# Performance work log

Measured on AMD Instinct MI355X. Metric: run time of the kernel, lower is better.

Reference implementation:

```python
import jax, jax.numpy as jnp
import numpy as np

CHUNK_SIZE = 256


def setup_inputs() -> dict:
    key = jax.random.key(0)
    kq, kk, kv = jax.random.split(key, 3)
    b, h, L, d, dv = 2, 16, 4096, 16, 64
    return {
        "q": jax.random.normal(kq, (b, h, L, d), dtype=jnp.float32),
        "k": jax.random.normal(kk, (b, h, L, d), dtype=jnp.float32),
        "v": jax.random.normal(kv, (b, h, L, dv), dtype=jnp.float32),
    }


def reference(q, k, v):
    b, h, L, d = q.shape
    dv = v.shape[-1]
    cs = CHUNK_SIZE
    n = L // cs

    q = q * d ** (-0.5)

    # ---- normalizer z over full sequence ----
    k_cumsum = jnp.cumsum(k, axis=-2)                               # [b,h,L,d]
    kk_cumsum = jnp.cumsum(k[..., :, None] * k[..., None, :], axis=-3)  # [b,h,L,d,d]
    z = (q * k_cumsum).sum(-1)
    z = z + 0.5 * jnp.einsum('bhld,bhle,bhlde->bhl', q, q, kk_cumsum)
    z = z + (jnp.arange(L, dtype=z.dtype) + 1.0)[None, None, :]

    # ---- zeroth-order term ----
    o_const = jnp.cumsum(v, axis=-2)                                # [b,h,L,dv]

    # ---- chunked view ----
    qc = q.reshape(b, h, n, cs, d)
    kc = k.reshape(b, h, n, cs, d)
    vc = v.reshape(b, h, n, cs, dv)

    # intra-chunk quadratic attention: S + 0.5*S^2, causal-masked
    s = jnp.einsum('bhnqd,bhnkd->bhnqk', qc, kc)                    # [b,h,n,cs,cs]
    s = s + 0.5 * s ** 2
    causal_mask = jnp.tril(jnp.ones((cs, cs), dtype=bool))
    s = jnp.where(causal_mask, s, jnp.zeros((), dtype=s.dtype))
    o = jnp.einsum('bhnqk,bhnkf->bhnqf', s, vc)                     # [b,h,n,cs,dv]

    # inter-chunk quadratic state: cumulative K x K x V from previous chunks
    kv_quad = jnp.einsum('bhncd,bhnce,bhncf->bhndef', kc, kc, vc)   # [b,h,n,d,d,dv]
    kv_quad = jnp.cumsum(kv_quad, axis=2)
    kv_quad = jnp.concatenate(
        [jnp.zeros_like(kv_quad[:, :, :1]), kv_quad[:, :, :-1]], axis=2)
    o = o + 0.5 * jnp.einsum('bhndef,bhncd,bhnce->bhncf', kv_quad, qc, qc)

    # inter-chunk linear state: cumulative K x V from previous chunks
    kv_lin = jnp.einsum('bhncd,bhnce->bhnde', kc, vc)               # [b,h,n,d,dv]
    kv_lin = jnp.cumsum(kv_lin, axis=2)
    kv_lin = jnp.concatenate(
        [jnp.zeros_like(kv_lin[:, :, :1]), kv_lin[:, :, :-1]], axis=2)
    o = o + jnp.einsum('bhnde,bhncd->bhnce', kv_lin, qc)

    o = o.reshape(b, h, L, dv) + o_const
    return o / (z[..., None] + 1e-6)
```

## Files before the change

kernel.cpp:

```cpp
#include <hip/hip_runtime.h>
#include <hip/hip_cooperative_groups.h>
#include <cstddef>

#define BH    32
#define LSEQ  4096
#define D     16
#define DV    64
#define CS    256
#define NC    16
#define NF    160
#define NZ    65
#define KSTEPS 5
#define PER   (NZ * NF)

typedef short short8 __attribute__((ext_vector_type(8)));
typedef float f32x4 __attribute__((ext_vector_type(4)));
typedef float f4 __attribute__((ext_vector_type(4)));
typedef unsigned uint4v __attribute__((ext_vector_type(4)));

#define OFF_KBF 0u
#define OFF_VT  (4u*1024u*1024u)
#define OFF_ST  (OFF_VT + (unsigned)(BH*NZ*LSEQ*2))

__device__ __forceinline__ unsigned f2bf(float x) {
  unsigned u = __float_as_uint(x);
  return (u + 0x7FFFu + ((u >> 16) & 1u)) >> 16;
}
__device__ __forceinline__ float bf2f(unsigned short u) {
  return __uint_as_float(((unsigned)u) << 16);
}
__device__ __forceinline__ short8 zero8() {
  short8 z = {0,0,0,0,0,0,0,0};
  return z;
}
__device__ __forceinline__ unsigned cvtpk(float lo, float hi) {
  unsigned r;
  asm("v_cvt_pk_bf16_f32 %0, %1, %2" : "=v"(r) : "v"(lo), "v"(hi));
  return r;
}
__device__ __forceinline__ short8 pk4(unsigned a, unsigned b, unsigned c, unsigned d) {
  uint4v u = {a, b, c, d};
  return __builtin_bit_cast(short8, u);
}

__device__ __forceinline__ unsigned feat_tbl(int f) {
  if (f == 0)  return 16u | (16u << 8);
  if (f <= 16) return (unsigned)(f - 1) | (16u << 8);
  if (f < 137) {
    int p = f - 17, off = 0;
    for (int d = 0; d < 15; ++d) {
      int cnt = 15 - d;
      if (p < off + cnt) return (unsigned)d | ((unsigned)(d + 1 + p - off) << 8);
      off += cnt;
    }
  }
  if (f < 153) {
    int d = f - 137;
    return (unsigned)d | ((unsigned)d << 8) | (1u << 16);
  }
  return 17u | (17u << 8);
}

struct Smem {
  float kxqx[CS][18];
  __align__(16) unsigned short vt[NZ][264];
  union {
    __align__(16) unsigned short stt[NZ][168];
    struct {
      __align__(16) unsigned short ptile[8][640];
      float zline[CS];
    } u;
  } b;
  unsigned tbl[NF];
};

__global__ __launch_bounds__(512, 4) void unified(const float* __restrict__ q,
                                                  const float* __restrict__ k,
                                                  const float* __restrict__ v,
                                                  unsigned* __restrict__ kbf_u32,
                                                  unsigned short* __restrict__ st,
                                                  float* __restrict__ out) {
  __shared__ Smem sm;
  int blk = blockIdx.x, bh = blk >> 4, c = blk & 15;
  int t = threadIdx.x, w = t >> 6, lane = t & 63, quad = lane >> 4, n16 = lane & 15;
  const size_t base = (size_t)bh * LSEQ + (size_t)c * CS;
  (void)kbf_u32;

  const int s0 = (w < 2) ? 2 * w : (w + 2);
  const int s1 = (w < 2) ? 2 * w + 1 : (17 - w);

  short8 qf[2] = {zero8(), zero8()};
  if (quad < 2) {
#pragma unroll
    for (int mm = 0; mm < 2; ++mm) {
      int s = mm ? s1 : s0;
      const f4* qp = (const f4*)(q + (base + (size_t)(s * 16 + n16)) * D + quad * 8);
      f4 qa = qp[0] * 0.25f;
      f4 qb = qp[1] * 0.25f;
      qf[mm] = pk4(cvtpk(qa[0], qa[1]), cvtpk(qa[2], qa[3]),
                   cvtpk(qb[0], qb[1]), cvtpk(qb[2], qb[3]));
    }
  }

  {
    const f4* K4 = (const f4*)(k + base * D);
    for (int idx = t; idx < 1024; idx += 512) {
      f4 kv = K4[idx];
      float* dst = &sm.kxqx[idx >> 2][(idx & 3) * 4];
      *(float2*)dst = make_float2(kv[0], kv[1]);
      *(float2*)(dst + 2) = make_float2(kv[2], kv[3]);
    }
    for (int i = t; i < CS; i += 512)
      *(float2*)&sm.kxqx[i][16] = make_float2(1.f, 0.f);
    const f4* V4 = (const f4*)(v + base * DV);
    for (int idx = t; idx < 2048; idx += 512) {
      int m16 = idx & 15, j0 = (idx >> 4) * 2;
      f4 a  = V4[j0 * 16 + m16];
      f4 bq = V4[j0 * 16 + 16 + m16];
#pragma unroll
      for (int r = 0; r < 4; ++r)
        *(unsigned*)&sm.vt[m16 * 4 + r][j0] = cvtpk(a[r], bq[r]);
    }
    if (t < 128) ((unsigned*)&sm.vt[64][0])[t] = 0x3F803F80u;
    if (t < NF) sm.tbl[t] = feat_tbl(t);
  }
  __syncthreads();

  if (c < 15) {
    const int ntt = (w < 2) ? 2 : 1;
    unsigned short* stc = st + (size_t)(bh * NC + c) * PER;
    for (int tt = 0; tt < ntt; ++tt) {
      const int T = tt ? (w + 8) : w;
      unsigned tv = sm.tbl[T * 16 + n16];
      int d0 = tv & 255, e0 = (tv >> 8) & 255;
      f32x4 acc5[5];
#pragma unroll
      for (int nt = 0; nt < 5; ++nt) acc5[nt] = (f32x4){0.f, 0.f, 0.f, 0.f};
      for (int jt = 0; jt < 8; ++jt) {
        float x[8];
#pragma unroll
        for (int i = 0; i < 8; ++i) {
          const float* kr = &sm.kxqx[jt * 32 + quad * 8 + i][0];
          x[i] = kr[d0] * kr[e0];
        }
        short8 afr = pk4(cvtpk(x[0], x[1]), cvtpk(x[2], x[3]),
                         cvtpk(x[4], x[5]), cvtpk(x[6], x[7]));
#pragma unroll
        for (int nt = 0; nt < 5; ++nt) {
          int ncol = nt * 16 + n16;
          short8 b = zero8();
          if (ncol < NZ) b = *(const short8*)(&sm.vt[ncol][jt * 32 + quad * 8]);
          acc5[nt] = __builtin_amdgcn_mfma_f32_16x16x32_bf16(afr, b, acc5[nt], 0, 0, 0);
        }
      }
      const int feat0 = T * 16 + quad * 4;
      float sc[4];
#pragma unroll
      for (int r = 0; r < 4; ++r)
        sc[r] = (feat0 + r >= 137 && feat0 + r < 153) ? 0.5f : 1.0f;
#pragma unroll
      for (int nt = 0; nt < 5; ++nt) {
        int col = nt * 16 + n16;
        if (col < NZ) {
          unsigned lo = cvtpk(acc5[nt][0] * sc[0], acc5[nt][1] * sc[1]);
          unsigned hi = cvtpk(acc5[nt][2] * sc[2], acc5[nt][3] * sc[3]);
          *(uint2*)(stc + (size_t)col * NF + feat0) = make_uint2(lo, hi);
        }
      }
    }
  }

  f32x4 accC[2][5];
#pragma unroll
  for (int mm = 0; mm < 2; ++mm)
#pragma unroll
    for (int nt = 0; nt < 5; ++nt) accC[mm][nt] = (f32x4){0.f, 0.f, 0.f, 0.f};

  {
    unsigned short* pw = &sm.b.u.ptile[w][0];
    short8 ones;
#pragma unroll
    for (int i = 0; i < 8; ++i) ones[i] = (short)0x3F80;

#pragma unroll
    for (int mm = 0; mm < 2; ++mm) {
      const int s = mm ? s1 : s0;
      const int ntiles = (s >> 1) + 1;
      for (int jt = 0; jt < ntiles; ++jt) {
        short8 kb[2];
#pragma unroll
        for (int ntk = 0; ntk < 2; ++ntk) {
          short8 b = zero8();
          if (quad < 2) {
            const float2* kr =
                (const float2*)&sm.kxqx[jt * 32 + ntk * 16 + n16][quad * 8];
            float2 k0 = kr[0], k1 = kr[1], k2 = kr[2], k3 = kr[3];
            b = pk4(cvtpk(k0.x, k0.y), cvtpk(k1.x, k1.y),
                    cvtpk(k2.x, k2.y), cvtpk(k3.x, k3.y));
          }
          kb[ntk] = b;
        }
        f32x4 zf = (f32x4){0.f, 0.f, 0.f, 0.f};
        f32x4 sres[2];
        sres[0] = __builtin_amdgcn_mfma_f32_16x16x32_bf16(qf[mm], kb[0], zf, 0, 0, 0);
        sres[1] = __builtin_amdgcn_mfma_f32_16x16x32_bf16(qf[mm], kb[1], zf, 0, 0, 0);
        const bool last = (jt == ntiles - 1);
#pragma unroll
        for (int ntk = 0; ntk < 2; ++ntk) {
          float ph[4];
#pragma unroll
          for (int r = 0; r < 4; ++r) {
            float sv = sres[ntk][r];
            float phi = fmaf(sv, fmaf(0.5f, sv, 1.0f), 1.0f);
            if (last) {
              int qrow_g = s * 16 + quad * 4 + r;
              int kcol_g = jt * 32 + ntk * 16 + n16;
              if (kcol_g > qrow_g) phi = 0.f;
            }
            ph[r] = phi;
          }
          unsigned u01 = cvtpk(ph[0], ph[1]);
          unsigned u23 = cvtpk(ph[2], ph[3]);
          int rb = (quad * 4) * 40 + ntk * 16 + n16;
          pw[rb      ] = (unsigned short)u01;
          pw[rb +  40] = (unsigned short)(u01 >> 16);
          pw[rb +  80] = (unsigned short)u23;
          pw[rb + 120] = (unsigned short)(u23 >> 16);
        }
        short8 pa = *(const short8*)(pw + n16 * 40 + quad * 8);
#pragma unroll
        for (int nt = 0; nt < 5; ++nt) {
          int ncol = nt * 16 + n16;
          short8 b;
          if (ncol < 64)       b = *(const short8*)(&sm.vt[ncol][jt * 32 + quad * 8]);
          else if (ncol == 64) b = ones;
          else                 b = zero8();
          accC[mm][nt] = __builtin_amdgcn_mfma_f32_16x16x32_bf16(pa, b, accC[mm][nt], 0, 0, 0);
        }
      }
    }
  }
  __syncthreads();

  {
    const f4* Q4 = (const f4*)(q + base * D);
    for (int idx = t; idx < 1024; idx += 512) {
      f4 qv = Q4[idx] * 0.25f;
      float* dst = &sm.kxqx[idx >> 2][(idx & 3) * 4];
      *(float2*)dst = make_float2(qv[0], qv[1]);
      *(float2*)(dst + 2) = make_float2(qv[2], qv[3]);
    }
  }

  cooperative_groups::this_grid().sync();

  if (c > 0) {
    const unsigned short* stg = st + (size_t)bh * NC * PER;
    float sa0[8], sa1[8], sa2[8];
#pragma unroll
    for (int e = 0; e < 8; ++e) { sa0[e] = 0.f; sa1[e] = 0.f; sa2[e] = 0.f; }
    const int i0 = t * 8, i1 = i0 + 4096, i2 = i0 + 8192;
    const bool h2 = (i2 < PER);
    short8 a0 = *(const short8*)(stg + i0);
    short8 a1 = *(const short8*)(stg + i1);
    short8 a2 = h2 ? *(const short8*)(stg + i2) : zero8();
    for (int cc = 1; cc < c; ++cc) {
      const unsigned short* pn = stg + (size_t)cc * PER;
      short8 b0 = *(const short8*)(pn + i0);
      short8 b1 = *(const short8*)(pn + i1);
      short8 b2 = h2 ? *(const short8*)(pn + i2) : zero8();
#pragma unroll
      for (int e = 0; e < 8; ++e) {
        sa0[e] += bf2f((unsigned short)a0[e]);
        sa1[e] += bf2f((unsigned short)a1[e]);
        sa2[e] += bf2f((unsigned short)a2[e]);
      }
      a0 = b0; a1 = b1; a2 = b2;
    }
#pragma unroll
    for (int e = 0; e < 8; ++e) {
      sa0[e] += bf2f((unsigned short)a0[e]);
      sa1[e] += bf2f((unsigned short)a1[e]);
      sa2[e] += bf2f((unsigned short)a2[e]);
    }
    {
      int col = i0 / NF, ft = i0 - col * NF;
      *(short8*)(&sm.b.stt[col][ft]) =
          pk4(cvtpk(sa0[0], sa0[1]), cvtpk(sa0[2], sa0[3]),
              cvtpk(sa0[4], sa0[5]), cvtpk(sa0[6], sa0[7]));
      col = i1 / NF; ft = i1 - col * NF;
      *(short8*)(&sm.b.stt[col][ft]) =
          pk4(cvtpk(sa1[0], sa1[1]), cvtpk(sa1[2], sa1[3]),
              cvtpk(sa1[4], sa1[5]), cvtpk(sa1[6], sa1[7]));
      if (h2) {
        col = i2 / NF; ft = i2 - col * NF;
        *(short8*)(&sm.b.stt[col][ft]) =
            pk4(cvtpk(sa2[0], sa2[1]), cvtpk(sa2[2], sa2[3]),
                cvtpk(sa2[4], sa2[5]), cvtpk(sa2[6], sa2[7]));
      }
    }
  }
  __syncthreads();

  if (c > 0) {
    const float* qrow0 = &sm.kxqx[s0 * 16 + n16][0];
    const float* qrow1 = &sm.kxqx[s1 * 16 + n16][0];
    for (int ks = 0; ks < KSTEPS; ++ks) {
      unsigned tvv[8];
#pragma unroll
      for (int i = 0; i < 8; ++i) tvv[i] = sm.tbl[ks * 32 + quad * 8 + i];
      float x0[8], x1[8];
#pragma unroll
      for (int i = 0; i < 8; ++i) {
        int d = tvv[i] & 255, e = (tvv[i] >> 8) & 255;
        x0[i] = qrow0[d] * qrow0[e];
        x1[i] = qrow1[d] * qrow1[e];
      }
      short8 afr0 = pk4(cvtpk(x0[0], x0[1]), cvtpk(x0[2], x0[3]),
                        cvtpk(x0[4], x0[5]), cvtpk(x0[6], x0[7]));
      short8 afr1 = pk4(cvtpk(x1[0], x1[1]), cvtpk(x1[2], x1[3]),
                        cvtpk(x1[4], x1[5]), cvtpk(x1[6], x1[7]));
#pragma unroll
      for (int nt = 0; nt < 5; ++nt) {
        int ncol = nt * 16 + n16;
        short8 b = zero8();
        if (ncol < NZ) b = *(const short8*)(&sm.b.stt[ncol][ks * 32 + quad * 8]);
        accC[0][nt] = __builtin_amdgcn_mfma_f32_16x16x32_bf16(afr0, b, accC[0][nt], 0, 0, 0);
        accC[1][nt] = __builtin_amdgcn_mfma_f32_16x16x32_bf16(afr1, b, accC[1][nt], 0, 0, 0);
      }
    }
  }
  __syncthreads();

  if (n16 == 0) {
#pragma unroll
    for (int mm = 0; mm < 2; ++mm) {
      int s = mm ? s1 : s0;
#pragma unroll
      for (int r = 0; r < 4; ++r)
        sm.b.u.zline[s * 16 + quad * 4 + r] = accC[mm][4][r];
    }
  }
  float* oc = out + base * DV;
#pragma unroll
  for (int mm = 0; mm < 2; ++mm) {
    int s = mm ? s1 : s0;
#pragma unroll
    for (int r = 0; r < 4; ++r) {
      int qrow = s * 16 + quad * 4 + r;
      float inv = __builtin_amdgcn_rcpf(sm.b.u.zline[qrow] + 1e-6f);
#pragma unroll
      for (int nt = 0; nt < 4; ++nt)
        oc[(size_t)qrow * DV + nt * 16 + n16] = accC[mm][nt][r] * inv;
    }
  }
}

__global__ __launch_bounds__(320) void pass_a(const float* __restrict__ k,
                                              const float* __restrict__ v,
                                              unsigned* __restrict__ kbf_u32,
                                              unsigned* __restrict__ vt_u32,
                                              unsigned short* __restrict__ st) {
  __shared__ float kx[CS][18];
  __shared__ __align__(16) unsigned short vt_lds[NZ][264];
  __shared__ unsigned tbl[NF];
  int blk = blockIdx.x, bh = blk >> 4, c = blk & 15;
  int t = threadIdx.x, w = t >> 6, lane = t & 63, quad = lane >> 4, n16 = lane & 15;
  {
    const float2* kc2 = (const float2*)(k + ((size_t)bh * LSEQ + c * CS) * D);
    unsigned* kbd = kbf_u32 + ((size_t)bh * LSEQ + c * CS) * D / 2;
    for (int i = t; i < 2048; i += 320) {
      float2 v2 = kc2[i];
      kbd[i] = f2bf(v2.x) | (f2bf(v2.y) << 16);
      int j = i >> 3, dd = (i & 7) * 2;
      kx[j][dd] = v2.x; kx[j][dd + 1] = v2.y;
    }
    for (int i = t; i < CS; i += 320) { kx[i][16] = 1.f; kx[i][17] = 0.f; }
  }
  {
    const float* vb = v + ((size_t)bh * LSEQ + c * CS) * DV;
    for (int i = t; i < CS * DV; i += 320) {
      int j = i >> 6, f = i & 63;
      vt_lds[f][j] = (unsigned short)f2bf(vb[i]);
    }
    for (int i = t; i < CS; i += 320) vt_lds[64][i] = (unsigned short)0x3F80;
  }
  if (t < NF) tbl[t] = feat_tbl(t);
  __syncthreads();
  {
    unsigned* vtg = vt_u32 + (size_t)bh * NZ * (LSEQ / 2) + c * (CS / 2);
    for (int i = t; i < NZ * (CS / 2); i += 320) {
      int f = i >> 7, jp = (i & 127) * 2;
      vtg[(size_t)f * (LSEQ / 2) + (i & 127)] =
          (unsigned)vt_lds[f][jp] | ((unsigned)vt_lds[f][jp + 1] << 16);
    }
  }
  f32x4 acc[2][5];
#pragma unroll
  for (int mm = 0; mm < 2; ++mm)
#pragma unroll
    for (int nt = 0; nt < 5; ++nt) acc[mm][nt] = (f32x4){0.f, 0.f, 0.f, 0.f};
  for (int jt = 0; jt < 8; ++jt) {
    short8 afr[2];
#pragma unroll
    for (int mm = 0; mm < 2; ++mm) {
      int feat = (w * 2 + mm) * 16 + n16;
      unsigned tv = tbl[feat];
      int d = tv & 255, e = (tv >> 8) & 255;
      short8 a;
#pragma unroll
      for (int i = 0; i < 8; ++i) {
        int jj = jt * 32 + quad * 8 + i;
        a[i] = (short)f2bf(kx[jj][d] * kx[jj][e]);
      }
      afr[mm] = a;
    }
#pragma unroll
    for (int nt = 0; nt < 5; ++nt) {
      int ncol = nt * 16 + n16;
      short8 b = zero8();
      if (ncol < NZ) b = *(const short8*)(&vt_lds[ncol][jt * 32 + quad * 8]);
      acc[0][nt] = __builtin_amdgcn_mfma_f32_16x16x32_bf16(afr[0], b, acc[0][nt], 0, 0, 0);
      acc[1][nt] = __builtin_amdgcn_mfma_f32_16x16x32_bf16(afr[1], b, acc[1][nt], 0, 0, 0);
    }
  }
  unsigned short* stc = st + (size_t)(bh * NC + c) * PER;
#pragma unroll
  for (int mm = 0; mm < 2; ++mm)
#pragma unroll
    for (int nt = 0; nt < 5; ++nt) {
      int col = nt * 16 + n16;
      if (col < NZ) {
        unsigned lo = f2bf(acc[mm][nt][0]) | (f2bf(acc[mm][nt][1]) << 16);
        unsigned hi = f2bf(acc[mm][nt][2]) | (f2bf(acc[mm][nt][3]) << 16);
        int feat0 = (w * 2 + mm) * 16 + quad * 4;
        *(uint2*)(stc + (size_t)col * NF + feat0) = make_uint2(lo, hi);
      }
    }
}

__global__ __launch_bounds__(256) void pass_b(unsigned short* __restrict__ st) {
  const int TOT = BH * PER;
  int idx = blockIdx.x * 256 + threadIdx.x;
  if (idx >= TOT) return;
  int bh = idx / PER, r = idx - bh * PER;
  unsigned short* p = st + (size_t)bh * NC * PER + r;
  float run = 0.f;
#pragma unroll
  for (int c = 0; c < NC; ++c) {
    unsigned short uv = p[(size_t)c * PER];
    float val = bf2f(uv);
    p[(size_t)c * PER] = (unsigned short)f2bf(run);
    run += val;
  }
}

__global__ __launch_bounds__(512) void pass_c(const float* __restrict__ q,
                                              const unsigned short* __restrict__ kbf,
                                              const unsigned short* __restrict__ vt,
                                              const unsigned short* __restrict__ st,
                                              float* __restrict__ out) {
  __shared__ float qx[CS][18];
  __shared__ unsigned tbl[NF];
  __shared__ __align__(16) unsigned short ptile[8][32 * 40];
  __shared__ float zline[CS];
  int blk = blockIdx.x, bh = blk >> 4, c = blk & 15;
  const size_t base = (size_t)bh * LSEQ + (size_t)c * CS;
  const float* qc = q + base * D;
  int t = threadIdx.x, w = t >> 6, lane = t & 63, quad = lane >> 4, n16 = lane & 15;
  for (int i = t; i < CS * D; i += 512) {
    int row = i >> 4, dd = i & 15;
    qx[row][dd] = qc[i] * 0.25f;
  }
  for (int i = t; i < CS; i += 512) { qx[i][16] = 1.f; qx[i][17] = 0.f; }
  if (t < NF) tbl[t] = feat_tbl(t);
  __syncthreads();
  f32x4 acc[2][5];
#pragma unroll
  for (int mm = 0; mm < 2; ++mm)
#pragma unroll
    for (int nt = 0; nt < 5; ++nt) acc[mm][nt] = (f32x4){0.f, 0.f, 0.f, 0.f};
  if (c > 0) {
    const unsigned short* stc = st + (size_t)(bh * NC + c) * PER;
    for (int ks = 0; ks < KSTEPS; ++ks) {
      short8 afr[2];
#pragma unroll
      for (int mm = 0; mm < 2; ++mm) {
        const float* qrow = qx[(w * 2 + mm) * 16 + n16];
        short8 a;
#pragma unroll
        for (int i = 0; i < 8; ++i) {
          int f = ks * 32 + quad * 8 + i;
          unsigned tv = tbl[f];
          float val = qrow[tv & 255] * qrow[(tv >> 8) & 255];
          if (tv & 0x10000u) val *= 0.5f;
          a[i] = (short)f2bf(val);
        }
        afr[mm] = a;
      }
#pragma unroll
      for (int nt = 0; nt < 5; ++nt) {
        int ncol = nt * 16 + n16;
        short8 b = zero8();
        if (ncol < NZ) b = *(const short8*)(stc + (size_t)ncol * NF + ks * 32 + quad * 8);
        acc[0][nt] = __builtin_amdgcn_mfma_f32_16x16x32_bf16(afr[0], b, acc[0][nt], 0, 0, 0);
        acc[1][nt] = __builtin_amdgcn_mfma_f32_16x16x32_bf16(afr[1], b, acc[1][nt], 0, 0, 0);
      }
    }
  }
  short8 qfr[2];
#pragma unroll
  for (int mm = 0; mm < 2; ++mm) {
    int m = (w * 2 + mm) * 16 + n16;
    short8 a = zero8();
    if (quad < 2) {
#pragma unroll
      for (int i = 0; i < 8; ++i) a[i] = (short)f2bf(qx[m][quad * 8 + i]);
    }
    qfr[mm] = a;
  }
  const unsigned short* kbc = kbf + base * D;
  const unsigned short* vtb = vt + (size_t)bh * NZ * LSEQ + (size_t)c * CS;
  unsigned short* pw = &ptile[w][0];
  short8 ones;
#pragma unroll
  for (int i = 0; i < 8; ++i) ones[i] = (short)0x3F80;
  for (int jt = 0; jt <= w; ++jt) {
    short8 kb[2];
#pragma unroll
    for (int ntk = 0; ntk < 2; ++ntk) {
      short8 b = zero8();
      if (quad < 2)
        b = *(const short8*)(kbc + (size_t)(jt * 32 + ntk * 16 + n16) * D + quad * 8);
      kb[ntk] = b;
    }
    f32x4 zf = (f32x4){0.f, 0.f, 0.f, 0.f};
    f32x4 s[2][2];
#pragma unroll
    for (int mm = 0; mm < 2; ++mm)
#pragma unroll
      for (int ntk = 0; ntk < 2; ++ntk)
        s[mm][ntk] = __builtin_amdgcn_mfma_f32_16x16x32_bf16(qfr[mm], kb[ntk], zf, 0, 0, 0);
    bool diag = (jt == w);
#pragma unroll
    for (int mm = 0; mm < 2; ++mm)
#pragma unroll
      for (int ntk = 0; ntk < 2; ++ntk)
#pragma unroll
        for (int r = 0; r < 4; ++r) {
          float sv = s[mm][ntk][r];
          float phi = fmaf(0.5f * sv, sv, sv) + 1.0f;
          if (diag) {
            int qrow = mm * 16 + quad * 4 + r;
            int kcol = ntk * 16 + n16;
            if (kcol > qrow) phi = 0.f;
          }
          pw[(mm * 16 + quad * 4 + r) * 40 + ntk * 16 + n16] = (unsigned short)f2bf(phi);
        }
    short8 pa[2];
#pragma unroll
    for (int mm = 0; mm < 2; ++mm)
      pa[mm] = *(const short8*)(pw + (mm * 16 + n16) * 40 + quad * 8);
#pragma unroll
    for (int nt = 0; nt < 5; ++nt) {
      int ncol = nt * 16 + n16;
      short8 b;
      if (ncol < 64)       b = *(const short8*)(vtb + (size_t)ncol * LSEQ + jt * 32 + quad * 8);
      else if (ncol == 64) b = ones;
      else                 b = zero8();
      acc[0][nt] = __builtin_amdgcn_mfma_f32_16x16x32_bf16(pa[0], b, acc[0][nt], 0, 0, 0);
      acc[1][nt] = __builtin_amdgcn_mfma_f32_16x16x32_bf16(pa[1], b, acc[1][nt], 0, 0, 0);
    }
  }
  if (n16 == 0) {
#pragma unroll
    for (int mm = 0; mm < 2; ++mm)
#pragma unroll
      for (int r = 0; r < 4; ++r)
        zline[(w * 2 + mm) * 16 + quad * 4 + r] = acc[mm][4][r];
  }
  float* oc = out + base * DV;
#pragma unroll
  for (int mm = 0; mm < 2; ++mm)
#pragma unroll
    for (int r = 0; r < 4; ++r) {
      int qrow = (w * 2 + mm) * 16 + quad * 4 + r;
      float inv = 1.0f / (zline[qrow] + 1e-6f);
#pragma unroll
      for (int nt = 0; nt < 4; ++nt)
        oc[(size_t)qrow * DV + nt * 16 + n16] = acc[mm][nt][r] * inv;
    }
}

extern "C" void kernel_launch(void* const* d_in, const int* in_sizes, int n_in,
                              void* d_out, int out_size, void* d_ws, size_t ws_size,
                              hipStream_t stream) {
  (void)in_sizes; (void)n_in; (void)out_size; (void)ws_size;
  const float* q = (const float*)d_in[0];
  const float* k = (const float*)d_in[1];
  const float* v = (const float*)d_in[2];
  float* out = (float*)d_out;
  char* wsb = (char*)d_ws;
  unsigned*       kbf32 = (unsigned*)(wsb + OFF_KBF);
  unsigned short* kbf   = (unsigned short*)(wsb + OFF_KBF);
  unsigned*       vt32  = (unsigned*)(wsb + OFF_VT);
  unsigned short* vtp   = (unsigned short*)(wsb + OFF_VT);
  unsigned short* stp   = (unsigned short*)(wsb + OFF_ST);

  int nb = 0;
  hipError_t oe = hipOccupancyMaxActiveBlocksPerMultiprocessor(
      &nb, reinterpret_cast<const void*>(unified), 512, 0);
  if (oe == hipSuccess && nb >= 2) {
    void* args[] = {(void*)&q, (void*)&k, (void*)&v,
                    (void*)&kbf32, (void*)&stp, (void*)&out};
    hipLaunchCooperativeKernel(reinterpret_cast<const void*>(unified),
                               dim3(BH * NC), dim3(512), args, 0, stream);
  } else {
    pass_a<<<BH * NC, 320, 0, stream>>>(k, v, kbf32, vt32, stp);
    pass_b<<<1300, 256, 0, stream>>>(stp);
    pass_c<<<BH * NC, 512, 0, stream>>>(q, kbf, vtp, stp, out);
  }
}
```

Baseline: 134.2 us.

## Replace cooperative grid-sync kernel with two plain launches for state and output

Splits the single cooperative kernel, which used a grid-wide sync, into two ordinary kernel launches. The first builds the per-chunk bf16 K copy and the quadratic/linear state contributions. The second loads Q and V, reads the prefix of states from earlier chunks, then runs the intra-chunk causal attention using global bf16 K. Block indexing changes to bh-minor so that chunks of one head are spread across launch order. This drops cooperative launch overhead and the grid barrier, at the cost of an extra launch and of re-reading V in the second kernel.

```diff
diff --git a/kernel.cpp b/kernel.cpp
--- a/kernel.cpp
+++ b/kernel.cpp
@@ -1,5 +1,4 @@
 #include <hip/hip_runtime.h>
-#include <hip/hip_cooperative_groups.h>
 #include <cstddef>
 
 #define BH    32
@@ -19,13 +18,8 @@
 typedef unsigned uint4v __attribute__((ext_vector_type(4)));
 
 #define OFF_KBF 0u
-#define OFF_VT  (4u*1024u*1024u)
-#define OFF_ST  (OFF_VT + (unsigned)(BH*NZ*LSEQ*2))
-
-__device__ __forceinline__ unsigned f2bf(float x) {
-  unsigned u = __float_as_uint(x);
-  return (u + 0x7FFFu + ((u >> 16) & 1u)) >> 16;
-}
+#define OFF_ST  (4u*1024u*1024u)
+
 __device__ __forceinline__ float bf2f(unsigned short u) {
   return __uint_as_float(((unsigned)u) << 16);
 }
@@ -61,8 +55,92 @@
   return 17u | (17u << 8);
 }
 
-struct Smem {
-  float kxqx[CS][18];
+__global__ __launch_bounds__(512, 4) void pass1(const float* __restrict__ k,
+                                                const float* __restrict__ v,
+                                                unsigned* __restrict__ kbf_u32,
+                                                unsigned short* __restrict__ st) {
+  __shared__ float kx[CS][18];
+  __shared__ __align__(16) unsigned short vt[NZ][264];
+  __shared__ unsigned tbl[NF];
+  int blk = blockIdx.x, bh = blk & 31, c = blk >> 5;
+  int t = threadIdx.x, w = t >> 6, lane = t & 63, quad = lane >> 4, n16 = lane & 15;
+  const size_t base = (size_t)bh * LSEQ + (size_t)c * CS;
+  (void)lane;
+
+  {
+    const f4* K4 = (const f4*)(k + base * D);
+    uint2* kbd2 = (uint2*)(kbf_u32 + base * D / 2);
+    for (int idx = t; idx < 1024; idx += 512) {
+      f4 kv = K4[idx];
+      kbd2[idx] = make_uint2(cvtpk(kv[0], kv[1]), cvtpk(kv[2], kv[3]));
+      float* dst = &kx[idx >> 2][(idx & 3) * 4];
+      *(float2*)dst = make_float2(kv[0], kv[1]);
+      *(float2*)(dst + 2) = make_float2(kv[2], kv[3]);
+    }
+    for (int i = t; i < CS; i += 512) { kx[i][16] = 1.f; kx[i][17] = 0.f; }
+  }
+  if (c < 15) {
+    const f4* V4 = (const f4*)(v + base * DV);
+    for (int idx = t; idx < 2048; idx += 512) {
+      int m16 = idx & 15, j0 = (idx >> 4) * 2;
+      f4 a  = V4[j0 * 16 + m16];
+      f4 bq = V4[j0 * 16 + 16 + m16];
+#pragma unroll
+      for (int r = 0; r < 4; ++r)
+        *(unsigned*)&vt[m16 * 4 + r][j0] = cvtpk(a[r], bq[r]);
+    }
+    if (t < 128) ((unsigned*)&vt[64][0])[t] = 0x3F803F80u;
+  }
+  if (t < NF) tbl[t] = feat_tbl(t);
+  __syncthreads();
+
+  if (c < 15) {
+    const int ntt = (w < 2) ? 2 : 1;
+    unsigned short* stc = st + (size_t)(bh * NC + c) * PER;
+    for (int tt = 0; tt < ntt; ++tt) {
+      const int T = tt ? (w + 8) : w;
+      unsigned tv = tbl[T * 16 + n16];
+      int d0 = tv & 255, e0 = (tv >> 8) & 255;
+      f32x4 acc5[5];
+#pragma unroll
+      for (int nt = 0; nt < 5; ++nt) acc5[nt] = (f32x4){0.f, 0.f, 0.f, 0.f};
+      for (int jt = 0; jt < 8; ++jt) {
+        float x[8];
+#pragma unroll
+        for (int i = 0; i < 8; ++i) {
+          const float* kr = &kx[jt * 32 + quad * 8 + i][0];
+          x[i] = kr[d0] * kr[e0];
+        }
+        short8 afr = pk4(cvtpk(x[0], x[1]), cvtpk(x[2], x[3]),
+                         cvtpk(x[4], x[5]), cvtpk(x[6], x[7]));
+#pragma unroll
+        for (int nt = 0; nt < 5; ++nt) {
+          int ncol = nt * 16 + n16;
+          short8 b = zero8();
+          if (ncol < NZ) b = *(const short8*)(&vt[ncol][jt * 32 + quad * 8]);
+          acc5[nt] = __builtin_amdgcn_mfma_f32_16x16x32_bf16(afr, b, acc5[nt], 0, 0, 0);
+        }
+      }
+      const int feat0 = T * 16 + quad * 4;
+      float sc[4];
+#pragma unroll
+      for (int r = 0; r < 4; ++r)
+        sc[r] = (feat0 + r >= 137 && feat0 + r < 153) ? 0.5f : 1.0f;
+#pragma unroll
+      for (int nt = 0; nt < 5; ++nt) {
+        int col = nt * 16 + n16;
+        if (col < NZ) {
+          unsigned lo = cvtpk(acc5[nt][0] * sc[0], acc5[nt][1] * sc[1]);
+          unsigned hi = cvtpk(acc5[nt][2] * sc[2], acc5[nt][3] * sc[3]);
+          *(uint2*)(stc + (size_t)col * NF + feat0) = make_uint2(lo, hi);
+        }
+      }
+    }
+  }
+}
+
+struct Smem2 {
+  float qx[CS][18];
   __align__(16) unsigned short vt[NZ][264];
   union {
     __align__(16) unsigned short stt[NZ][168];
@@ -74,17 +152,15 @@
   unsigned tbl[NF];
 };
 
-__global__ __launch_bounds__(512, 4) void unified(const float* __restrict__ q,
-                                                  const float* __restrict__ k,
-                                                  const float* __restrict__ v,
-                                                  unsigned* __restrict__ kbf_u32,
-                                                  unsigned short* __restrict__ st,
-                                                  float* __restrict__ out) {
-  __shared__ Smem sm;
-  int blk = blockIdx.x, bh = blk >> 4, c = blk & 15;
+__global__ __launch_bounds__(512, 4) void pass2(const float* __restrict__ q,
+                                                const unsigned short* __restrict__ kbf,
+                                                const float* __restrict__ v,
+                                                const unsigned short* __restrict__ st,
+                                                float* __restrict__ out) {
+  __shared__ Smem2 sm;
+  int blk = blockIdx.x, bh = blk & 31, c = blk >> 5;
   int t = threadIdx.x, w = t >> 6, lane = t & 63, quad = lane >> 4, n16 = lane & 15;
   const size_t base = (size_t)bh * LSEQ + (size_t)c * CS;
-  (void)kbf_u32;
 
   const int s0 = (w < 2) ? 2 * w : (w + 2);
   const int s1 = (w < 2) ? 2 * w + 1 : (17 - w);
@@ -103,15 +179,14 @@
   }
 
   {
-    const f4* K4 = (const f4*)(k + base * D);
+    const f4* Q4 = (const f4*)(q + base * D);
     for (int idx = t; idx < 1024; idx += 512) {
-      f4 kv = K4[idx];
-      float* dst = &sm.kxqx[idx >> 2][(idx & 3) * 4];
-      *(float2*)dst = make_float2(kv[0], kv[1]);
-      *(float2*)(dst + 2) = make_float2(kv[2], kv[3]);
-    }
-    for (int i = t; i < CS; i += 512)
-      *(float2*)&sm.kxqx[i][16] = make_float2(1.f, 0.f);
+      f4 qv = Q4[idx] * 0.25f;
+      float* dst = &sm.qx[idx >> 2][(idx & 3) * 4];
+      *(float2*)dst = make_float2(qv[0], qv[1]);
+      *(float2*)(dst + 2) = make_float2(qv[2], qv[3]);
+    }
+    for (int i = t; i < CS; i += 512) { sm.qx[i][16] = 1.f; sm.qx[i][17] = 0.f; }
     const f4* V4 = (const f4*)(v + base * DV);
     for (int idx = t; idx < 2048; idx += 512) {
       int m16 = idx & 15, j0 = (idx >> 4) * 2;
@@ -125,134 +200,6 @@
     if (t < NF) sm.tbl[t] = feat_tbl(t);
   }
   __syncthreads();
-
-  if (c < 15) {
-    const int ntt = (w < 2) ? 2 : 1;
-    unsigned short* stc = st + (size_t)(bh * NC + c) * PER;
-    for (int tt = 0; tt < ntt; ++tt) {
-      const int T = tt ? (w + 8) : w;
-      unsigned tv = sm.tbl[T * 16 + n16];
-      int d0 = tv & 255, e0 = (tv >> 8) & 255;
-      f32x4 acc5[5];
-#pragma unroll
-      for (int nt = 0; nt < 5; ++nt) acc5[nt] = (f32x4){0.f, 0.f, 0.f, 0.f};
-      for (int jt = 0; jt < 8; ++jt) {
-        float x[8];
-#pragma unroll
-        for (int i = 0; i < 8; ++i) {
-          const float* kr = &sm.kxqx[jt * 32 + quad * 8 + i][0];
-          x[i] = kr[d0] * kr[e0];
-        }
-        short8 afr = pk4(cvtpk(x[0], x[1]), cvtpk(x[2], x[3]),
-                         cvtpk(x[4], x[5]), cvtpk(x[6], x[7]));
-#pragma unroll
-        for (int nt = 0; nt < 5; ++nt) {
-          int ncol = nt * 16 + n16;
-          short8 b = zero8();
-          if (ncol < NZ) b = *(const short8*)(&sm.vt[ncol][jt * 32 + quad * 8]);
-          acc5[nt] = __builtin_amdgcn_mfma_f32_16x16x32_bf16(afr, b, acc5[nt], 0, 0, 0);
-        }
-      }
-      const int feat0 = T * 16 + quad * 4;
-      float sc[4];
-#pragma unroll
-      for (int r = 0; r < 4; ++r)
-        sc[r] = (feat0 + r >= 137 && feat0 + r < 153) ? 0.5f : 1.0f;
-#pragma unroll
-      for (int nt = 0; nt < 5; ++nt) {
-        int col = nt * 16 + n16;
-        if (col < NZ) {
-          unsigned lo = cvtpk(acc5[nt][0] * sc[0], acc5[nt][1] * sc[1]);
-          unsigned hi = cvtpk(acc5[nt][2] * sc[2], acc5[nt][3] * sc[3]);
-          *(uint2*)(stc + (size_t)col * NF + feat0) = make_uint2(lo, hi);
-        }
-      }
-    }
-  }
-
-  f32x4 accC[2][5];
-#pragma unroll
-  for (int mm = 0; mm < 2; ++mm)
-#pragma unroll
-    for (int nt = 0; nt < 5; ++nt) accC[mm][nt] = (f32x4){0.f, 0.f, 0.f, 0.f};
-
-  {
-    unsigned short* pw = &sm.b.u.ptile[w][0];
-    short8 ones;
-#pragma unroll
-    for (int i = 0; i < 8; ++i) ones[i] = (short)0x3F80;
-
-#pragma unroll
-    for (int mm = 0; mm < 2; ++mm) {
-      const int s = mm ? s1 : s0;
-      const int ntiles = (s >> 1) + 1;
-      for (int jt = 0; jt < ntiles; ++jt) {
-        short8 kb[2];
-#pragma unroll
-        for (int ntk = 0; ntk < 2; ++ntk) {
-          short8 b = zero8();
-          if (quad < 2) {
-            const float2* kr =
-                (const float2*)&sm.kxqx[jt * 32 + ntk * 16 + n16][quad * 8];
-            float2 k0 = kr[0], k1 = kr[1], k2 = kr[2], k3 = kr[3];
-            b = pk4(cvtpk(k0.x, k0.y), cvtpk(k1.x, k1.y),
-                    cvtpk(k2.x, k2.y), cvtpk(k3.x, k3.y));
-          }
-          kb[ntk] = b;
-        }
-        f32x4 zf = (f32x4){0.f, 0.f, 0.f, 0.f};
-        f32x4 sres[2];
-        sres[0] = __builtin_amdgcn_mfma_f32_16x16x32_bf16(qf[mm], kb[0], zf, 0, 0, 0);
-        sres[1] = __builtin_amdgcn_mfma_f32_16x16x32_bf16(qf[mm], kb[1], zf, 0, 0, 0);
-        const bool last = (jt == ntiles - 1);
-#pragma unroll
-        for (int ntk = 0; ntk < 2; ++ntk) {
-          float ph[4];
-#pragma unroll
-          for (int r = 0; r < 4; ++r) {
-            float sv = sres[ntk][r];
-            float phi = fmaf(sv, fmaf(0.5f, sv, 1.0f), 1.0f);
-            if (last) {
-              int qrow_g = s * 16 + quad * 4 + r;
-              int kcol_g = jt * 32 + ntk * 16 + n16;
-              if (kcol_g > qrow_g) phi = 0.f;
-            }
-            ph[r] = phi;
-          }
-          unsigned u01 = cvtpk(ph[0], ph[1]);
-          unsigned u23 = cvtpk(ph[2], ph[3]);
-          int rb = (quad * 4) * 40 + ntk * 16 + n16;
-          pw[rb      ] = (unsigned short)u01;
-          pw[rb +  40] = (unsigned short)(u01 >> 16);
-          pw[rb +  80] = (unsigned short)u23;
-          pw[rb + 120] = (unsigned short)(u23 >> 16);
-        }
-        short8 pa = *(const short8*)(pw + n16 * 40 + quad * 8);
-#pragma unroll
-        for (int nt = 0; nt < 5; ++nt) {
-          int ncol = nt * 16 + n16;
-          short8 b;
-          if (ncol < 64)       b = *(const short8*)(&sm.vt[ncol][jt * 32 + quad * 8]);
-          else if (ncol == 64) b = ones;
-          else                 b = zero8();
-          accC[mm][nt] = __builtin_amdgcn_mfma_f32_16x16x32_bf16(pa, b, accC[mm][nt], 0, 0, 0);
-        }
-      }
-    }
-  }
-  __syncthreads();
-
-  {
-    const f4* Q4 = (const f4*)(q + base * D);
-    for (int idx = t; idx < 1024; idx += 512) {
-      f4 qv = Q4[idx] * 0.25f;
-      float* dst = &sm.kxqx[idx >> 2][(idx & 3) * 4];
-      *(float2*)dst = make_float2(qv[0], qv[1]);
-      *(float2*)(dst + 2) = make_float2(qv[2], qv[3]);
-    }
-  }
-
-  cooperative_groups::this_grid().sync();
 
   if (c > 0) {
     const unsigned short* stg = st + (size_t)bh * NC * PER;
@@ -302,9 +249,15 @@
   }
   __syncthreads();
 
+  f32x4 accC[2][5];
+#pragma unroll
+  for (int mm = 0; mm < 2; ++mm)
+#pragma unroll
+    for (int nt = 0; nt < 5; ++nt) accC[mm][nt] = (f32x4){0.f, 0.f, 0.f, 0.f};
+
   if (c > 0) {
-    const float* qrow0 = &sm.kxqx[s0 * 16 + n16][0];
-    const float* qrow1 = &sm.kxqx[s1 * 16 + n16][0];
+    const float* qrow0 = &sm.qx[s0 * 16 + n16][0];
+    const float* qrow1 = &sm.qx[s1 * 16 + n16][0];
     for (int ks = 0; ks < KSTEPS; ++ks) {
       unsigned tvv[8];
 #pragma unroll
@@ -332,6 +285,65 @@
   }
   __syncthreads();
 
+  const unsigned short* kbc = kbf + base * D;
+  unsigned short* pw = &sm.b.u.ptile[w][0];
+  short8 ones;
+#pragma unroll
+  for (int i = 0; i < 8; ++i) ones[i] = (short)0x3F80;
+
+#pragma unroll
+  for (int mm = 0; mm < 2; ++mm) {
+    const int s = mm ? s1 : s0;
+    const int ntiles = (s >> 1) + 1;
+    for (int jt = 0; jt < ntiles; ++jt) {
+      short8 kb[2];
+#pragma unroll
+      for (int ntk = 0; ntk < 2; ++ntk) {
+        short8 b = zero8();
+        if (quad < 2)
+          b = *(const short8*)(kbc + (size_t)(jt * 32 + ntk * 16 + n16) * D + quad * 8);
+        kb[ntk] = b;
+      }
+      f32x4 zf = (f32x4){0.f, 0.f, 0.f, 0.f};
+      f32x4 sres[2];
+      sres[0] = __builtin_amdgcn_mfma_f32_16x16x32_bf16(qf[mm], kb[0], zf, 0, 0, 0);
+      sres[1] = __builtin_amdgcn_mfma_f32_16x16x32_bf16(qf[mm], kb[1], zf, 0, 0, 0);
+      const bool last = (jt == ntiles - 1);
+#pragma unroll
+      for (int ntk = 0; ntk < 2; ++ntk) {
+        float ph[4];
+#pragma unroll
+        for (int r = 0; r < 4; ++r) {
+          float sv = sres[ntk][r];
+          float phi = fmaf(sv, fmaf(0.5f, sv, 1.0f), 1.0f);
+          if (last) {
+            int qrow_g = s * 16 + quad * 4 + r;
+            int kcol_g = jt * 32 + ntk * 16 + n16;
+            if (kcol_g > qrow_g) phi = 0.f;
+          }
+          ph[r] = phi;
+        }
+        unsigned u01 = cvtpk(ph[0], ph[1]);
+        unsigned u23 = cvtpk(ph[2], ph[3]);
+        int rb = (quad * 4) * 40 + ntk * 16 + n16;
+        pw[rb      ] = (unsigned short)u01;
+        pw[rb +  40] = (unsigned short)(u01 >> 16);
+        pw[rb +  80] = (unsigned short)u23;
+        pw[rb + 120] = (unsigned short)(u23 >> 16);
+      }
+      short8 pa = *(const short8*)(pw + n16 * 40 + quad * 8);
+#pragma unroll
+      for (int nt = 0; nt < 5; ++nt) {
+        int ncol = nt * 16 + n16;
+        short8 b;
+        if (ncol < 64)       b = *(const short8*)(&sm.vt[ncol][jt * 32 + quad * 8]);
+        else if (ncol == 64) b = ones;
+        else                 b = zero8();
+        accC[mm][nt] = __builtin_amdgcn_mfma_f32_16x16x32_bf16(pa, b, accC[mm][nt], 0, 0, 0);
+      }
+    }
+  }
+
   if (n16 == 0) {
 #pragma unroll
     for (int mm = 0; mm < 2; ++mm) {
@@ -354,242 +366,6 @@
         oc[(size_t)qrow * DV + nt * 16 + n16] = accC[mm][nt][r] * inv;
     }
   }
-}
-
-__global__ __launch_bounds__(320) void pass_a(const float* __restrict__ k,
-                                              const float* __restrict__ v,
-                                              unsigned* __restrict__ kbf_u32,
-                                              unsigned* __restrict__ vt_u32,
-                                              unsigned short* __restrict__ st) {
-  __shared__ float kx[CS][18];
-  __shared__ __align__(16) unsigned short vt_lds[NZ][264];
-  __shared__ unsigned tbl[NF];
-  int blk = blockIdx.x, bh = blk >> 4, c = blk & 15;
-  int t = threadIdx.x, w = t >> 6, lane = t & 63, quad = lane >> 4, n16 = lane & 15;
-  {
-    const float2* kc2 = (const float2*)(k + ((size_t)bh * LSEQ + c * CS) * D);
-    unsigned* kbd = kbf_u32 + ((size_t)bh * LSEQ + c * CS) * D / 2;
-    for (int i = t; i < 2048; i += 320) {
-      float2 v2 = kc2[i];
-      kbd[i] = f2bf(v2.x) | (f2bf(v2.y) << 16);
-      int j = i >> 3, dd = (i & 7) * 2;
-      kx[j][dd] = v2.x; kx[j][dd + 1] = v2.y;
-    }
-    for (int i = t; i < CS; i += 320) { kx[i][16] = 1.f; kx[i][17] = 0.f; }
-  }
-  {
-    const float* vb = v + ((size_t)bh * LSEQ + c * CS) * DV;
-    for (int i = t; i < CS * DV; i += 320) {
-      int j = i >> 6, f = i & 63;
-      vt_lds[f][j] = (unsigned short)f2bf(vb[i]);
-    }
-    for (int i = t; i < CS; i += 320) vt_lds[64][i] = (unsigned short)0x3F80;
-  }
-  if (t < NF) tbl[t] = feat_tbl(t);
-  __syncthreads();
-  {
-    unsigned* vtg = vt_u32 + (size_t)bh * NZ * (LSEQ / 2) + c * (CS / 2);
-    for (int i = t; i < NZ * (CS / 2); i += 320) {
-      int f = i >> 7, jp = (i & 127) * 2;
-      vtg[(size_t)f * (LSEQ / 2) + (i & 127)] =
-          (unsigned)vt_lds[f][jp] | ((unsigned)vt_lds[f][jp + 1] << 16);
-    }
-  }
-  f32x4 acc[2][5];
-#pragma unroll
-  for (int mm = 0; mm < 2; ++mm)
-#pragma unroll
-    for (int nt = 0; nt < 5; ++nt) acc[mm][nt] = (f32x4){0.f, 0.f, 0.f, 0.f};
-  for (int jt = 0; jt < 8; ++jt) {
-    short8 afr[2];
-#pragma unroll
-    for (int mm = 0; mm < 2; ++mm) {
-      int feat = (w * 2 + mm) * 16 + n16;
-      unsigned tv = tbl[feat];
-      int d = tv & 255, e = (tv >> 8) & 255;
-      short8 a;
-#pragma unroll
-      for (int i = 0; i < 8; ++i) {
-        int jj = jt * 32 + quad * 8 + i;
-        a[i] = (short)f2bf(kx[jj][d] * kx[jj][e]);
-      }
-      afr[mm] = a;
-    }
-#pragma unroll
-    for (int nt = 0; nt < 5; ++nt) {
-      int ncol = nt * 16 + n16;
-      short8 b = zero8();
-      if (ncol < NZ) b = *(const short8*)(&vt_lds[ncol][jt * 32 + quad * 8]);
-      acc[0][nt] = __builtin_amdgcn_mfma_f32_16x16x32_bf16(afr[0], b, acc[0][nt], 0, 0, 0);
-      acc[1][nt] = __builtin_amdgcn_mfma_f32_16x16x32_bf16(afr[1], b, acc[1][nt], 0, 0, 0);
-    }
-  }
-  unsigned short* stc = st + (size_t)(bh * NC + c) * PER;
-#pragma unroll
-  for (int mm = 0; mm < 2; ++mm)
-#pragma unroll
-    for (int nt = 0; nt < 5; ++nt) {
-      int col = nt * 16 + n16;
-      if (col < NZ) {
-        unsigned lo = f2bf(acc[mm][nt][0]) | (f2bf(acc[mm][nt][1]) << 16);
-        unsigned hi = f2bf(acc[mm][nt][2]) | (f2bf(acc[mm][nt][3]) << 16);
-        int feat0 = (w * 2 + mm) * 16 + quad * 4;
-        *(uint2*)(stc + (size_t)col * NF + feat0) = make_uint2(lo, hi);
-      }
-    }
-}
-
-__global__ __launch_bounds__(256) void pass_b(unsigned short* __restrict__ st) {
-  const int TOT = BH * PER;
-  int idx = blockIdx.x * 256 + threadIdx.x;
-  if (idx >= TOT) return;
-  int bh = idx / PER, r = idx - bh * PER;
-  unsigned short* p = st + (size_t)bh * NC * PER + r;
-  float run = 0.f;
-#pragma unroll
-  for (int c = 0; c < NC; ++c) {
-    unsigned short uv = p[(size_t)c * PER];
-    float val = bf2f(uv);
-    p[(size_t)c * PER] = (unsigned short)f2bf(run);
-    run += val;
-  }
-}
-
-__global__ __launch_bounds__(512) void pass_c(const float* __restrict__ q,
-                                              const unsigned short* __restrict__ kbf,
-                                              const unsigned short* __restrict__ vt,
-                                              const unsigned short* __restrict__ st,
-                                              float* __restrict__ out) {
-  __shared__ float qx[CS][18];
-  __shared__ unsigned tbl[NF];
-  __shared__ __align__(16) unsigned short ptile[8][32 * 40];
-  __shared__ float zline[CS];
-  int blk = blockIdx.x, bh = blk >> 4, c = blk & 15;
-  const size_t base = (size_t)bh * LSEQ + (size_t)c * CS;
-  const float* qc = q + base * D;
-  int t = threadIdx.x, w = t >> 6, lane = t & 63, quad = lane >> 4, n16 = lane & 15;
-  for (int i = t; i < CS * D; i += 512) {
-    int row = i >> 4, dd = i & 15;
-    qx[row][dd] = qc[i] * 0.25f;
-  }
-  for (int i = t; i < CS; i += 512) { qx[i][16] = 1.f; qx[i][17] = 0.f; }
-  if (t < NF) tbl[t] = feat_tbl(t);
-  __syncthreads();
-  f32x4 acc[2][5];
-#pragma unroll
-  for (int mm = 0; mm < 2; ++mm)
-#pragma unroll
-    for (int nt = 0; nt < 5; ++nt) acc[mm][nt] = (f32x4){0.f, 0.f, 0.f, 0.f};
-  if (c > 0) {
-    const unsigned short* stc = st + (size_t)(bh * NC + c) * PER;
-    for (int ks = 0; ks < KSTEPS; ++ks) {
-      short8 afr[2];
-#pragma unroll
-      for (int mm = 0; mm < 2; ++mm) {
-        const float* qrow = qx[(w * 2 + mm) * 16 + n16];
-        short8 a;
-#pragma unroll
-        for (int i = 0; i < 8; ++i) {
-          int f = ks * 32 + quad * 8 + i;
-          unsigned tv = tbl[f];
-          float val = qrow[tv & 255] * qrow[(tv >> 8) & 255];
-          if (tv & 0x10000u) val *= 0.5f;
-          a[i] = (short)f2bf(val);
-        }
-        afr[mm] = a;
-      }
-#pragma unroll
-      for (int nt = 0; nt < 5; ++nt) {
-        int ncol = nt * 16 + n16;
-        short8 b = zero8();
-        if (ncol < NZ) b = *(const short8*)(stc + (size_t)ncol * NF + ks * 32 + quad * 8);
-        acc[0][nt] = __builtin_amdgcn_mfma_f32_16x16x32_bf16(afr[0], b, acc[0][nt], 0, 0, 0);
-        acc[1][nt] = __builtin_amdgcn_mfma_f32_16x16x32_bf16(afr[1], b, acc[1][nt], 0, 0, 0);
-      }
-    }
-  }
-  short8 qfr[2];
-#pragma unroll
-  for (int mm = 0; mm < 2; ++mm) {
-    int m = (w * 2 + mm) * 16 + n16;
-    short8 a = zero8();
-    if (quad < 2) {
-#pragma unroll
-      for (int i = 0; i < 8; ++i) a[i] = (short)f2bf(qx[m][quad * 8 + i]);
-    }
-    qfr[mm] = a;
-  }
-  const unsigned short* kbc = kbf + base * D;
-  const unsigned short* vtb = vt + (size_t)bh * NZ * LSEQ + (size_t)c * CS;
-  unsigned short* pw = &ptile[w][0];
-  short8 ones;
-#pragma unroll
-  for (int i = 0; i < 8; ++i) ones[i] = (short)0x3F80;
-  for (int jt = 0; jt <= w; ++jt) {
-    short8 kb[2];
-#pragma unroll
-    for (int ntk = 0; ntk < 2; ++ntk) {
-      short8 b = zero8();
-      if (quad < 2)
-        b = *(const short8*)(kbc + (size_t)(jt * 32 + ntk * 16 + n16) * D + quad * 8);
-      kb[ntk] = b;
-    }
-    f32x4 zf = (f32x4){0.f, 0.f, 0.f, 0.f};
-    f32x4 s[2][2];
-#pragma unroll
-    for (int mm = 0; mm < 2; ++mm)
-#pragma unroll
-      for (int ntk = 0; ntk < 2; ++ntk)
-        s[mm][ntk] = __builtin_amdgcn_mfma_f32_16x16x32_bf16(qfr[mm], kb[ntk], zf, 0, 0, 0);
-    bool diag = (jt == w);
-#pragma unroll
-    for (int mm = 0; mm < 2; ++mm)
-#pragma unroll
-      for (int ntk = 0; ntk < 2; ++ntk)
-#pragma unroll
-        for (int r = 0; r < 4; ++r) {
-          float sv = s[mm][ntk][r];
-          float phi = fmaf(0.5f * sv, sv, sv) + 1.0f;
-          if (diag) {
-            int qrow = mm * 16 + quad * 4 + r;
-            int kcol = ntk * 16 + n16;
-            if (kcol > qrow) phi = 0.f;
-          }
-          pw[(mm * 16 + quad * 4 + r) * 40 + ntk * 16 + n16] = (unsigned short)f2bf(phi);
-        }
-    short8 pa[2];
-#pragma unroll
-    for (int mm = 0; mm < 2; ++mm)
-      pa[mm] = *(const short8*)(pw + (mm * 16 + n16) * 40 + quad * 8);
-#pragma unroll
-    for (int nt = 0; nt < 5; ++nt) {
-      int ncol = nt * 16 + n16;
-      short8 b;
-      if (ncol < 64)       b = *(const short8*)(vtb + (size_t)ncol * LSEQ + jt * 32 + quad * 8);
-      else if (ncol == 64) b = ones;
-      else                 b = zero8();
-      acc[0][nt] = __builtin_amdgcn_mfma_f32_16x16x32_bf16(pa[0], b, acc[0][nt], 0, 0, 0);
-      acc[1][nt] = __builtin_amdgcn_mfma_f32_16x16x32_bf16(pa[1], b, acc[1][nt], 0, 0, 0);
-    }
-  }
-  if (n16 == 0) {
-#pragma unroll
-    for (int mm = 0; mm < 2; ++mm)
-#pragma unroll
-      for (int r = 0; r < 4; ++r)
-        zline[(w * 2 + mm) * 16 + quad * 4 + r] = acc[mm][4][r];
-  }
-  float* oc = out + base * DV;
-#pragma unroll
-  for (int mm = 0; mm < 2; ++mm)
-#pragma unroll
-    for (int r = 0; r < 4; ++r) {
-      int qrow = (w * 2 + mm) * 16 + quad * 4 + r;
-      float inv = 1.0f / (zline[qrow] + 1e-6f);
-#pragma unroll
-      for (int nt = 0; nt < 4; ++nt)
-        oc[(size_t)qrow * DV + nt * 16 + n16] = acc[mm][nt][r] * inv;
-    }
 }
 
 extern "C" void kernel_launch(void* const* d_in, const int* in_sizes, int n_in,
@@ -603,21 +379,8 @@
   char* wsb = (char*)d_ws;
   unsigned*       kbf32 = (unsigned*)(wsb + OFF_KBF);
   unsigned short* kbf   = (unsigned short*)(wsb + OFF_KBF);
-  unsigned*       vt32  = (unsigned*)(wsb + OFF_VT);
-  unsigned short* vtp   = (unsigned short*)(wsb + OFF_VT);
   unsigned short* stp   = (unsigned short*)(wsb + OFF_ST);
 
-  int nb = 0;
-  hipError_t oe = hipOccupancyMaxActiveBlocksPerMultiprocessor(
-      &nb, reinterpret_cast<const void*>(unified), 512, 0);
-  if (oe == hipSuccess && nb >= 2) {
-    void* args[] = {(void*)&q, (void*)&k, (void*)&v,
-                    (void*)&kbf32, (void*)&stp, (void*)&out};
-    hipLaunchCooperativeKernel(reinterpret_cast<const void*>(unified),
-                               dim3(BH * NC), dim3(512), args, 0, stream);
-  } else {
-    pass_a<<<BH * NC, 320, 0, stream>>>(k, v, kbf32, vt32, stp);
-    pass_b<<<1300, 256, 0, stream>>>(stp);
-    pass_c<<<BH * NC, 512, 0, stream>>>(q, kbf, vtp, stp, out);
-  }
-}
+  pass1<<<BH * NC, 512, 0, stream>>>(k, v, kbf32, stp);
+  pass2<<<BH * NC, 512, 0, stream>>>(q, kbf, v, stp, out);
+}
```

New measurement: 126.4 us. 1.06x faster.
